# Kernel optimization log

Measured on AMD Instinct MI355X. Metric: run time of the kernel, lower is better.

Reference implementation:

```python
import jax, jax.numpy as jnp
import numpy as np

B, M_IN, H, W = 8, 63, 480, 640
VALID_FRAC = 0.05  # sparse-depth valid pixel density
N_ITERS = 5


def setup_inputs() -> dict:
    key = jax.random.key(0)
    k1, k2, k3 = jax.random.split(key, 3)
    bases = jax.random.normal(k1, (B, M_IN, H, W), dtype=jnp.float32)
    logit = jax.random.normal(k2, (B, 1, H, W), dtype=jnp.float32)
    valid = jax.random.uniform(k3, (B, 1, H, W)) < VALID_FRAC
    # invalid sparse-depth pixels -> log(0) = -inf, ignored via isfinite mask
    targets = jnp.where(valid, logit, -jnp.inf)
    return {"bases": bases, "targets": targets}


def _fit_single(basis, target):
    # basis: (m,h,w), target: (1,h,w)
    m = basis.shape[0]
    y = target[0]                                   # (h,w)
    mask = jnp.isfinite(y)
    maskf = mask.astype(basis.dtype)
    Xf = (basis * maskf).reshape(m, -1)             # masked basis, (m, hw)
    yf = jnp.where(mask, y, 0.0).reshape(-1)        # (hw,)
    XtX = Xf @ Xf.T                                 # (m,m) over valid pixels only
    Xty = Xf @ yf                                   # (m,)
    N = maskf.sum()

    # eval-mode EM-like refinement (prior.use == False): Tr_d = M / beta
    beta0 = jnp.sqrt(N)
    beta = beta0
    done = jnp.array(False)
    for _ in range(N_ITERS):
        w = jnp.linalg.solve(XtX * beta, Xty * beta)    # LU solve
        E_d = jnp.sum((yf - w @ Xf) ** 2)               # residual on valid pixels
        Tr_d = m / beta
        beta_new = N / (E_d + Tr_d)
        conv = jnp.abs(beta_new / beta0 - 1.0) < 0.02
        beta = jnp.where(done, beta, beta_new)
        beta0 = jnp.where(done, beta0, beta_new)
        done = done | conv

    A = XtX * beta
    w = jnp.linalg.solve(A, Xty * beta)                 # (m,)

    # recon3d: predicted log depth
    logit_pred = jnp.einsum('m,mhw->hw', w, basis)[None]  # (1,h,w)

    # pred_var: S_inv via Cholesky, var = (S_inv @ bt * bt).sum(0)
    L = jnp.linalg.cholesky(A)
    S_inv = jax.scipy.linalg.cho_solve((L, True), jnp.eye(m, dtype=basis.dtype))
    bt = basis.reshape(m, -1)                           # (m, hw)
    var = jnp.sum((S_inv @ bt) * bt, axis=0).reshape(1, basis.shape[1], basis.shape[2])
    return logit_pred, w, var


def reference(bases, targets):
    # th_homogenize(append=False): prepend a constant ones basis channel
    ones = jnp.ones_like(bases[:, :1])
    basis_h = jnp.concatenate([ones, bases], axis=1)    # (b, m+1, h, w)
    logits, weights, logit_var = jax.vmap(_fit_single)(basis_h, targets)
    return logits, weights, logit_var
```

## Files before the change

### kernel.cpp

```cpp
#include <hip/hip_runtime.h>
#include <cmath>

#define HW 307200
#define NB 8
#define NBASE 63
#define NCHUNK (HW/256)
#define GRAM_BLKS 128
#define QCAP 320

#define XTY_OFF 0
#define YTY_OFF (NB*64)
#define NC_OFF  (YTY_OFF + NB)
#define ZERO_FLOATS (NC_OFF + NB)
#define XTX_OFF ZERO_FLOATS
#define MP_OFF  (XTX_OFF + NB*64*64)
#define WV_OFF  (MP_OFF + NB*64*64)

#define OUT_W   (NB*HW)
#define OUT_VAR (OUT_W + NB*64)

__device__ __forceinline__ bool finitef(float x) {
    return (__float_as_uint(x) & 0x7f800000u) != 0x7f800000u;
}

__global__ __launch_bounds__(256) void gram_kernel(
    const float* __restrict__ bases, const float* __restrict__ targets,
    float* __restrict__ ws, float* __restrict__ part)
{
    __shared__ float tile[64*68];
    __shared__ float sy[64];
    __shared__ float qy[QCAP];
    __shared__ int   qidx[QCAP];
    __shared__ int   qn;

    const int t  = threadIdx.x;
    const int b  = blockIdx.y;
    const int wv = t >> 6;
    const int l  = t & 63;
    const int ti = l >> 3, tj = l & 7;

    float acc[8][8];
#pragma unroll
    for (int i = 0; i < 8; i++)
#pragma unroll
        for (int j = 0; j < 8; j++) acc[i][j] = 0.f;
    float acc_xty = 0.f, acc_yty = 0.f, acc_n = 0.f;

    const float* __restrict__ basesb = bases + (long)b * NBASE * HW;
    const float* __restrict__ targb  = targets + (long)b * HW;
    const long choff = (long)(l - 1) * HW;

    if (t == 0) qn = 0;
    __syncthreads();

    auto compute_tile = [&]() {
#pragma unroll 2
        for (int pp = 0; pp < 16; ++pp) {
            const int p2 = wv * 16 + pp;
            const float4 r0 = *(const float4*)&tile[p2*68 + 8*ti];
            const float4 r1 = *(const float4*)&tile[p2*68 + 8*ti + 4];
            const float4 c0 = *(const float4*)&tile[p2*68 + 8*tj];
            const float4 c1 = *(const float4*)&tile[p2*68 + 8*tj + 4];
            const float rr[8] = {r0.x,r0.y,r0.z,r0.w,r1.x,r1.y,r1.z,r1.w};
            const float cc[8] = {c0.x,c0.y,c0.z,c0.w,c1.x,c1.y,c1.z,c1.w};
#pragma unroll
            for (int i = 0; i < 8; i++)
#pragma unroll
                for (int j = 0; j < 8; j++)
                    acc[i][j] = fmaf(rr[i], cc[j], acc[i][j]);
            acc_xty = fmaf(sy[p2], tile[p2*68 + l], acc_xty);
        }
    };

    int qtot = 0;
    for (int j = blockIdx.x; j < NCHUNK; j += GRAM_BLKS) {
        const int p = j * 256 + t;
        const float y = targb[p];
        const bool fin = finitef(y);
        const unsigned long long m = __ballot(fin);
        int wbase = 0;
        if (l == 0) wbase = atomicAdd(&qn, __popcll(m));
        wbase = __shfl(wbase, 0, 64);
        if (fin) {
            const int r = __popcll(m & ((1ull << l) - 1ull));
            qidx[wbase + r] = p;
            qy[wbase + r]   = y;
            acc_yty = fmaf(y, y, acc_yty);
            acc_n += 1.f;
        }
        __syncthreads();
        qtot = qn;
        while (qtot >= 64) {
            const int base = qtot - 64;
            if (t < 64) sy[t] = qy[base + t];
#pragma unroll
            for (int pp = wv; pp < 64; pp += 4) {
                const int gp = qidx[base + pp];
                float v;
                if (l == 0) v = 1.f;
                else        v = basesb[choff + gp];
                tile[pp*68 + l] = v;
            }
            __syncthreads();
            compute_tile();
            qtot -= 64;
            __syncthreads();
        }
        if (t == 0) qn = qtot;
        __syncthreads();
    }

    if (qtot > 0) {
        if (t < 64) sy[t] = (t < qtot) ? qy[t] : 0.f;
#pragma unroll
        for (int pp = wv; pp < 64; pp += 4) {
            float v = 0.f;
            if (pp < qtot) {
                const int gp = qidx[pp];
                if (l == 0) v = 1.f;
                else        v = basesb[choff + gp];
            }
            tile[pp*68 + l] = v;
        }
        __syncthreads();
        compute_tile();
    }
    __syncthreads();

    for (int w = 0; w < 4; ++w) {
        if (wv == w) {
#pragma unroll
            for (int i = 0; i < 8; i++)
#pragma unroll
                for (int j2 = 0; j2 < 8; j2++) {
                    const int e = (8*ti + i) * 64 + 8*tj + j2;
                    tile[e] = (w == 0) ? acc[i][j2] : tile[e] + acc[i][j2];
                }
        }
        __syncthreads();
    }
    float* __restrict__ pb = part + (long)(b * GRAM_BLKS + blockIdx.x) * 4096;
#pragma unroll
    for (int k = 0; k < 4; ++k)
        *(float4*)&pb[t*16 + 4*k] = *(const float4*)&tile[t*16 + 4*k];

    for (int w = 0; w < 4; ++w) {
        if (wv == w) tile[4096 + l] = (w == 0) ? acc_xty : tile[4096 + l] + acc_xty;
        __syncthreads();
    }
    if (t < 64) atomicAdd(&ws[XTY_OFF + b*64 + t], tile[4096 + t]);

#pragma unroll
    for (int off = 32; off; off >>= 1) {
        acc_yty += __shfl_down(acc_yty, off, 64);
        acc_n   += __shfl_down(acc_n,   off, 64);
    }
    if (l == 0) {
        atomicAdd(&ws[YTY_OFF + b], acc_yty);
        atomicAdd(&ws[NC_OFF  + b], acc_n);
    }
}

__global__ __launch_bounds__(256) void reduce_kernel(
    const float* __restrict__ part, float* __restrict__ ws)
{
    const int b = blockIdx.y;
    const int e = blockIdx.x * 256 + threadIdx.x;
    const float* __restrict__ pb = part + (long)b * GRAM_BLKS * 4096 + e;
    float s = 0.f;
#pragma unroll 8
    for (int k = 0; k < GRAM_BLKS; ++k)
        s += pb[(long)k * 4096];
    ws[XTX_OFF + b*4096 + e] = s;
}

__global__ __launch_bounds__(256) void solve_kernel(
    float* __restrict__ ws, float* __restrict__ out)
{
    __shared__ float A[64*65];
    __shared__ float W[64*65];
    __shared__ float d0[64], xty_s[64], wv_s[64];
    __shared__ float ib_s;

    const int b = blockIdx.x;
    const int t = threadIdx.x;
    const int r = t & 63;
    const int q = t >> 6;
    const float* XtX = ws + XTX_OFF + b * 4096;

    for (int e = t; e < 4096; e += 256)
        A[(e >> 6) * 65 + (e & 63)] = XtX[e];
    if (t < 64) xty_s[t] = ws[XTY_OFF + b*64 + t];
    const float yty = ws[YTY_OFF + b];
    const float Nc  = ws[NC_OFF  + b];
    __syncthreads();
    if (t < 64) d0[t] = A[t*65 + t];
    __syncthreads();

    for (int k = 0; k < 64; k++) {
        const float akk = A[k*65 + k];
        __syncthreads();
        const float dk = sqrtf(akk);
        if (q == 0) {
            if (r == k)     A[k*65 + k] = dk;
            else if (r > k) A[r*65 + k] /= dk;
        }
        __syncthreads();
        if (r > k) {
            const float lrk = A[r*65 + k];
            for (int j = k + 1 + q; j <= r; j += 4)
                A[r*65 + j] -= lrk * A[j*65 + k];
        }
        __syncthreads();
    }

    if (q == 0) {
        for (int i = 0; i < 64; i++) {
            float s = (i == r) ? 1.f : 0.f;
            for (int j = 0; j < i; j++) s = fmaf(-A[i*65 + j], W[j*65 + r], s);
            W[i*65 + r] = s / A[i*65 + i];
        }
        for (int i = 63; i >= 0; i--) {
            float s = W[i*65 + r];
            for (int j = i + 1; j < 64; j++) s = fmaf(-A[j*65 + i], W[j*65 + r], s);
            W[i*65 + r] = s / A[i*65 + i];
        }
        float wt = 0.f;
        for (int j = 0; j < 64; j++) wt = fmaf(W[r*65 + j], xty_s[j], wt);
        wv_s[r] = wt;

        float qt = 0.f;
        for (int j = 0; j < 64; j++) {
            float x = (j > r) ? A[r*65 + j] : ((j == r) ? d0[r] : A[j*65 + r]);
            qt = fmaf(x, wv_s[j], qt);
        }
        float r1 = wt * xty_s[r];
        float r2 = wt * qt;
#pragma unroll
        for (int off = 32; off; off >>= 1) {
            r1 += __shfl_down(r1, off, 64);
            r2 += __shfl_down(r2, off, 64);
        }
        if (r == 0) {
            const float E_d = yty - 2.f * r1 + r2;
            float beta0 = sqrtf(Nc);
            float beta  = beta0;
            bool  done  = false;
#pragma unroll
            for (int it = 0; it < 5; ++it) {
                float Tr_d = 64.f / beta;
                float beta_new = Nc / (E_d + Tr_d);
                bool conv = fabsf(beta_new / beta0 - 1.f) < 0.02f;
                if (!done) { beta = beta_new; beta0 = beta_new; }
                done = done || conv;
            }
            ib_s = 1.f / beta;
        }
        out[OUT_W + b*64 + r] = wt;
        ws[WV_OFF + b*64 + r] = wt;
    }
    __syncthreads();

    const float ib = ib_s;
    float* __restrict__ Mp = ws + MP_OFF + b * 4096;
    for (int e = t; e < 4096; e += 256) {
        const int row = e >> 6, j = e & 63;
        const float v = (j < row) ? 0.f
                      : ((j == row) ? 0.5f : 1.f) * W[row*65 + j] * ib;
        Mp[e] = v;
    }
}

__global__ __launch_bounds__(256, 2) void predvar_kernel(
    const float* __restrict__ bases, const float* __restrict__ ws,
    float* __restrict__ out)
{
    __shared__ float Mp_s[4096];
    __shared__ float w_s[64];

    const int b = blockIdx.y;
    const int t = threadIdx.x;
    {
        const float4* __restrict__ src = (const float4*)(ws + MP_OFF + b * 4096);
        float4* dst = (float4*)Mp_s;
        for (int e = t; e < 1024; e += 256) dst[e] = src[e];
        if (t < 64) w_s[t] = ws[WV_OFF + b*64 + t];
    }
    __syncthreads();

    const int pix = (blockIdx.x * 256 + t) * 2;
    const float* basesb = bases + (long)b * NBASE * HW + pix;

    float2 bv[64];
    bv[0] = make_float2(1.f, 1.f);
#pragma unroll
    for (int c = 1; c < 64; c++)
        bv[c] = *(const float2*)&basesb[(long)(c - 1) * HW];

    float px = w_s[0], py = w_s[0];
#pragma unroll
    for (int c = 1; c < 64; c++) {
        px = fmaf(w_s[c], bv[c].x, px);
        py = fmaf(w_s[c], bv[c].y, py);
    }

    float vx = 0.f, vy = 0.f;
#pragma unroll
    for (int i = 0; i < 64; i++) {
        float sx = 0.f, sy2 = 0.f;
#pragma unroll
        for (int qd = i >> 2; qd < 16; qd++) {
            const float4 m = *(const float4*)&Mp_s[i*64 + 4*qd];
            sx  = fmaf(m.x, bv[4*qd+0].x, sx);
            sy2 = fmaf(m.x, bv[4*qd+0].y, sy2);
            sx  = fmaf(m.y, bv[4*qd+1].x, sx);
            sy2 = fmaf(m.y, bv[4*qd+1].y, sy2);
            sx  = fmaf(m.z, bv[4*qd+2].x, sx);
            sy2 = fmaf(m.z, bv[4*qd+2].y, sy2);
            sx  = fmaf(m.w, bv[4*qd+3].x, sx);
            sy2 = fmaf(m.w, bv[4*qd+3].y, sy2);
        }
        vx = fmaf(sx,  bv[i].x, vx);
        vy = fmaf(sy2, bv[i].y, vy);
    }

    *(float2*)&out[(long)b * HW + pix] = make_float2(px, py);
    *(float2*)&out[OUT_VAR + (long)b * HW + pix] = make_float2(2.f * vx, 2.f * vy);
}

extern "C" void kernel_launch(void* const* d_in, const int* in_sizes, int n_in,
                              void* d_out, int out_size, void* d_ws, size_t ws_size,
                              hipStream_t stream)
{
    const float* bases   = (const float*)d_in[0];
    const float* targets = (const float*)d_in[1];
    float* out = (float*)d_out;
    float* ws  = (float*)d_ws;

    hipMemsetAsync(d_ws, 0, ZERO_FLOATS * sizeof(float), stream);

    gram_kernel<<<dim3(GRAM_BLKS, NB), 256, 0, stream>>>(bases, targets, ws, out);
    reduce_kernel<<<dim3(16, NB), 256, 0, stream>>>(out, ws);
    solve_kernel<<<NB, 256, 0, stream>>>(ws, out);
    predvar_kernel<<<dim3(HW / 512, NB), 256, 0, stream>>>(bases, ws, out);
}
```

Measured before the change: 578.3 us.

## Gather valid pixels in 16-pixel groups and keep inverse columns in registers

The Gram kernel no longer compacts individual valid pixels. It queues 16-pixel groups that contain at least one valid pixel and loads all 16 pixels per channel, multiplying by a 0/1 mask. This gives contiguous 64-byte reads instead of scattered 4-byte ones, at the cost of loading and multiplying many masked-out pixels (about 44% of groups hold a valid pixel at 5% density). The solve kernel drops to 64 threads, each holding one inverse column in registers, with unrolled four-way-accumulated triangular solves. It also writes Mp transposed, which removes the W shared array and several barriers.

```diff
diff --git a/kernel.cpp b/kernel.cpp
--- a/kernel.cpp
+++ b/kernel.cpp
@@ -6,7 +6,7 @@
 #define NBASE 63
 #define NCHUNK (HW/256)
 #define GRAM_BLKS 128
-#define QCAP 320
+#define GQCAP 24
 
 #define XTY_OFF 0
 #define YTY_OFF (NB*64)
@@ -29,8 +29,9 @@
 {
     __shared__ float tile[64*68];
     __shared__ float sy[64];
-    __shared__ float qy[QCAP];
-    __shared__ int   qidx[QCAP];
+    __shared__ float sm[64];
+    __shared__ int   qg[GQCAP];
+    __shared__ int   qmsk[GQCAP];
     __shared__ int   qn;
 
     const int t  = threadIdx.x;
@@ -48,7 +49,6 @@
 
     const float* __restrict__ basesb = bases + (long)b * NBASE * HW;
     const float* __restrict__ targb  = targets + (long)b * HW;
-    const long choff = (long)(l - 1) * HW;
 
     if (t == 0) qn = 0;
     __syncthreads();
@@ -72,58 +72,88 @@
         }
     };
 
-    int qtot = 0;
+    auto gather_group = [&](int gi) {
+        const int pl  = l & 15;
+        const int ch4 = l >> 4;
+        const float mf = sm[wv*16 + pl];
+        const float* __restrict__ gp = basesb + (long)gi * 16 + pl;
+#pragma unroll
+        for (int q = 0; q < 16; q++) {
+            const int c = q*4 + ch4;
+            float v;
+            if (c == 0) v = mf;
+            else        v = gp[(long)(c - 1) * HW] * mf;
+            tile[(wv*16 + pl)*68 + c] = v;
+        }
+    };
+    auto zero_group_rows = [&]() {
+        const int pl  = l & 15;
+        const int ch4 = l >> 4;
+#pragma unroll
+        for (int q = 0; q < 16; q++)
+            tile[(wv*16 + pl)*68 + q*4 + ch4] = 0.f;
+    };
+
     for (int j = blockIdx.x; j < NCHUNK; j += GRAM_BLKS) {
         const int p = j * 256 + t;
         const float y = targb[p];
         const bool fin = finitef(y);
+        if (fin) { acc_yty = fmaf(y, y, acc_yty); acc_n += 1.f; }
         const unsigned long long m = __ballot(fin);
-        int wbase = 0;
-        if (l == 0) wbase = atomicAdd(&qn, __popcll(m));
-        wbase = __shfl(wbase, 0, 64);
-        if (fin) {
-            const int r = __popcll(m & ((1ull << l) - 1ull));
-            qidx[wbase + r] = p;
-            qy[wbase + r]   = y;
-            acc_yty = fmaf(y, y, acc_yty);
-            acc_n += 1.f;
-        }
-        __syncthreads();
-        qtot = qn;
-        while (qtot >= 64) {
-            const int base = qtot - 64;
-            if (t < 64) sy[t] = qy[base + t];
-#pragma unroll
-            for (int pp = wv; pp < 64; pp += 4) {
-                const int gp = qidx[base + pp];
-                float v;
-                if (l == 0) v = 1.f;
-                else        v = basesb[choff + gp];
-                tile[pp*68 + l] = v;
+        if ((l & 15) == 0) {
+            const unsigned gm = (unsigned)((m >> l) & 0xFFFFull);
+            if (gm) {
+                const int pos = atomicAdd(&qn, 1);
+                qg[pos]   = p >> 4;
+                qmsk[pos] = (int)gm;
+            }
+        }
+        __syncthreads();
+        int nq = qn;
+        while (nq >= 4) {
+            const int base = nq - 4;
+            if (t < 64) {
+                const int gsel = t >> 4;
+                const int gi   = qg[base + gsel];
+                const int msk  = qmsk[base + gsel];
+                const int pix  = gi*16 + (t & 15);
+                const float yv = targb[pix];
+                const bool v   = (msk >> (t & 15)) & 1;
+                sm[t] = v ? 1.f : 0.f;
+                sy[t] = v ? yv : 0.f;
             }
             __syncthreads();
+            gather_group(qg[base + wv]);
+            __syncthreads();
             compute_tile();
-            qtot -= 64;
+            nq = base;
             __syncthreads();
         }
-        if (t == 0) qn = qtot;
-        __syncthreads();
-    }
-
-    if (qtot > 0) {
-        if (t < 64) sy[t] = (t < qtot) ? qy[t] : 0.f;
-#pragma unroll
-        for (int pp = wv; pp < 64; pp += 4) {
-            float v = 0.f;
-            if (pp < qtot) {
-                const int gp = qidx[pp];
-                if (l == 0) v = 1.f;
-                else        v = basesb[choff + gp];
+        if (t == 0) qn = nq;
+        __syncthreads();
+    }
+
+    {
+        const int nq = qn;
+        if (nq > 0) {
+            if (t < 64) {
+                const int gsel = t >> 4;
+                if (gsel < nq) {
+                    const int gi  = qg[gsel];
+                    const int msk = qmsk[gsel];
+                    const int pix = gi*16 + (t & 15);
+                    const float yv = targb[pix];
+                    const bool v   = (msk >> (t & 15)) & 1;
+                    sm[t] = v ? 1.f : 0.f;
+                    sy[t] = v ? yv : 0.f;
+                } else { sm[t] = 0.f; sy[t] = 0.f; }
             }
-            tile[pp*68 + l] = v;
-        }
-        __syncthreads();
-        compute_tile();
+            __syncthreads();
+            if (wv < nq) gather_group(qg[wv]);
+            else         zero_group_rows();
+            __syncthreads();
+            compute_tile();
+        }
     }
     __syncthreads();
 
@@ -174,100 +204,129 @@
     ws[XTX_OFF + b*4096 + e] = s;
 }
 
-__global__ __launch_bounds__(256) void solve_kernel(
+__global__ __launch_bounds__(64) void solve_kernel(
     float* __restrict__ ws, float* __restrict__ out)
 {
     __shared__ float A[64*65];
-    __shared__ float W[64*65];
-    __shared__ float d0[64], xty_s[64], wv_s[64];
-    __shared__ float ib_s;
+    __shared__ float d0[64], dinv_s[64], xty_s[64], wv_s[64];
 
     const int b = blockIdx.x;
     const int t = threadIdx.x;
-    const int r = t & 63;
-    const int q = t >> 6;
     const float* XtX = ws + XTX_OFF + b * 4096;
 
-    for (int e = t; e < 4096; e += 256)
+    for (int e = t; e < 4096; e += 64)
         A[(e >> 6) * 65 + (e & 63)] = XtX[e];
-    if (t < 64) xty_s[t] = ws[XTY_OFF + b*64 + t];
+    xty_s[t] = ws[XTY_OFF + b*64 + t];
     const float yty = ws[YTY_OFF + b];
     const float Nc  = ws[NC_OFF  + b];
     __syncthreads();
-    if (t < 64) d0[t] = A[t*65 + t];
+    d0[t] = A[t*65 + t];
     __syncthreads();
 
     for (int k = 0; k < 64; k++) {
         const float akk = A[k*65 + k];
         __syncthreads();
         const float dk = sqrtf(akk);
-        if (q == 0) {
-            if (r == k)     A[k*65 + k] = dk;
-            else if (r > k) A[r*65 + k] /= dk;
-        }
-        __syncthreads();
-        if (r > k) {
-            const float lrk = A[r*65 + k];
-            for (int j = k + 1 + q; j <= r; j += 4)
-                A[r*65 + j] -= lrk * A[j*65 + k];
-        }
-        __syncthreads();
-    }
-
-    if (q == 0) {
-        for (int i = 0; i < 64; i++) {
-            float s = (i == r) ? 1.f : 0.f;
-            for (int j = 0; j < i; j++) s = fmaf(-A[i*65 + j], W[j*65 + r], s);
-            W[i*65 + r] = s / A[i*65 + i];
-        }
-        for (int i = 63; i >= 0; i--) {
-            float s = W[i*65 + r];
-            for (int j = i + 1; j < 64; j++) s = fmaf(-A[j*65 + i], W[j*65 + r], s);
-            W[i*65 + r] = s / A[i*65 + i];
-        }
-        float wt = 0.f;
-        for (int j = 0; j < 64; j++) wt = fmaf(W[r*65 + j], xty_s[j], wt);
-        wv_s[r] = wt;
-
-        float qt = 0.f;
-        for (int j = 0; j < 64; j++) {
-            float x = (j > r) ? A[r*65 + j] : ((j == r) ? d0[r] : A[j*65 + r]);
-            qt = fmaf(x, wv_s[j], qt);
-        }
-        float r1 = wt * xty_s[r];
-        float r2 = wt * qt;
-#pragma unroll
-        for (int off = 32; off; off >>= 1) {
-            r1 += __shfl_down(r1, off, 64);
-            r2 += __shfl_down(r2, off, 64);
-        }
-        if (r == 0) {
-            const float E_d = yty - 2.f * r1 + r2;
-            float beta0 = sqrtf(Nc);
-            float beta  = beta0;
-            bool  done  = false;
-#pragma unroll
-            for (int it = 0; it < 5; ++it) {
-                float Tr_d = 64.f / beta;
-                float beta_new = Nc / (E_d + Tr_d);
-                bool conv = fabsf(beta_new / beta0 - 1.f) < 0.02f;
-                if (!done) { beta = beta_new; beta0 = beta_new; }
-                done = done || conv;
-            }
-            ib_s = 1.f / beta;
-        }
-        out[OUT_W + b*64 + r] = wt;
-        ws[WV_OFF + b*64 + r] = wt;
-    }
-    __syncthreads();
-
-    const float ib = ib_s;
+        if (t == k)      A[k*65 + k] = dk;
+        else if (t > k)  A[t*65 + k] /= dk;
+        __syncthreads();
+        if (t > k) {
+            const float ltk = A[t*65 + k];
+            for (int j = k + 1; j <= t; j++)
+                A[t*65 + j] -= ltk * A[j*65 + k];
+        }
+        __syncthreads();
+    }
+
+    dinv_s[t] = 1.f / A[t*65 + t];
+    __syncthreads();
+
+    float Wc[64];
+#pragma unroll
+    for (int i = 0; i < 64; i++) {
+        float s0 = (i == t) ? 1.f : 0.f, s1 = 0.f, s2 = 0.f, s3 = 0.f;
+        const int nfull = i >> 2;
+#pragma unroll
+        for (int qd = 0; qd < nfull; qd++) {
+            const int j = qd * 4;
+            s0 = fmaf(-A[i*65 + j    ], Wc[j    ], s0);
+            s1 = fmaf(-A[i*65 + j + 1], Wc[j + 1], s1);
+            s2 = fmaf(-A[i*65 + j + 2], Wc[j + 2], s2);
+            s3 = fmaf(-A[i*65 + j + 3], Wc[j + 3], s3);
+        }
+#pragma unroll
+        for (int j = nfull * 4; j < i; j++)
+            s0 = fmaf(-A[i*65 + j], Wc[j], s0);
+        Wc[i] = ((s0 + s1) + (s2 + s3)) * dinv_s[i];
+    }
+#pragma unroll
+    for (int i = 63; i >= 0; i--) {
+        float s0 = Wc[i], s1 = 0.f, s2 = 0.f, s3 = 0.f;
+        const int j0 = i + 1;
+        const int nfull = (64 - j0) >> 2;
+#pragma unroll
+        for (int qd = 0; qd < nfull; qd++) {
+            const int j = j0 + qd * 4;
+            s0 = fmaf(-A[(j    )*65 + i], Wc[j    ], s0);
+            s1 = fmaf(-A[(j + 1)*65 + i], Wc[j + 1], s1);
+            s2 = fmaf(-A[(j + 2)*65 + i], Wc[j + 2], s2);
+            s3 = fmaf(-A[(j + 3)*65 + i], Wc[j + 3], s3);
+        }
+#pragma unroll
+        for (int j = j0 + nfull * 4; j < 64; j++)
+            s0 = fmaf(-A[j*65 + i], Wc[j], s0);
+        Wc[i] = ((s0 + s1) + (s2 + s3)) * dinv_s[i];
+    }
+
+    float w0 = 0.f, w1 = 0.f, w2 = 0.f, w3 = 0.f;
+#pragma unroll
+    for (int j = 0; j < 64; j += 4) {
+        w0 = fmaf(Wc[j    ], xty_s[j    ], w0);
+        w1 = fmaf(Wc[j + 1], xty_s[j + 1], w1);
+        w2 = fmaf(Wc[j + 2], xty_s[j + 2], w2);
+        w3 = fmaf(Wc[j + 3], xty_s[j + 3], w3);
+    }
+    const float wt = (w0 + w1) + (w2 + w3);
+    wv_s[t] = wt;
+    __syncthreads();
+
+    float qt = 0.f;
+#pragma unroll
+    for (int j = 0; j < 64; j++) {
+        const float x = (j > t) ? A[t*65 + j] : ((j == t) ? d0[t] : A[j*65 + t]);
+        qt = fmaf(x, wv_s[j], qt);
+    }
+    float r1 = wt * xty_s[t];
+    float r2 = wt * qt;
+#pragma unroll
+    for (int off = 32; off; off >>= 1) {
+        r1 += __shfl_down(r1, off, 64);
+        r2 += __shfl_down(r2, off, 64);
+    }
+    r1 = __shfl(r1, 0, 64);
+    r2 = __shfl(r2, 0, 64);
+    const float E_d = yty - 2.f * r1 + r2;
+
+    float beta0 = sqrtf(Nc);
+    float beta  = beta0;
+    bool  done  = false;
+#pragma unroll
+    for (int it = 0; it < 5; ++it) {
+        const float Tr_d = 64.f / beta;
+        const float beta_new = Nc / (E_d + Tr_d);
+        const bool conv = fabsf(beta_new / beta0 - 1.f) < 0.02f;
+        if (!done) { beta = beta_new; beta0 = beta_new; }
+        done = done || conv;
+    }
+    const float ib = 1.f / beta;
+
+    out[OUT_W + b*64 + t] = wt;
+    ws[WV_OFF + b*64 + t] = wt;
     float* __restrict__ Mp = ws + MP_OFF + b * 4096;
-    for (int e = t; e < 4096; e += 256) {
-        const int row = e >> 6, j = e & 63;
-        const float v = (j < row) ? 0.f
-                      : ((j == row) ? 0.5f : 1.f) * W[row*65 + j] * ib;
-        Mp[e] = v;
+#pragma unroll
+    for (int j = 0; j < 64; j++) {
+        const float v = (j > t) ? 0.f : ((j == t) ? 0.5f : 1.f) * Wc[j] * ib;
+        Mp[j*64 + t] = v;
     }
 }
 
@@ -341,6 +400,6 @@
 
     gram_kernel<<<dim3(GRAM_BLKS, NB), 256, 0, stream>>>(bases, targets, ws, out);
     reduce_kernel<<<dim3(16, NB), 256, 0, stream>>>(out, ws);
-    solve_kernel<<<NB, 256, 0, stream>>>(ws, out);
+    solve_kernel<<<NB, 64, 0, stream>>>(ws, out);
     predvar_kernel<<<dim3(HW / 512, NB), 256, 0, stream>>>(bases, ws, out);
 }
```

Result: slower. 621.4 us (+7.4%).
